# Kernel optimization log

Measured on AMD Instinct MI355X. Metric: run time of the kernel, lower is better.

## Reference

```python
import jax, jax.numpy as jnp
import numpy as np

B, D, H, W = 1, 16, 16, 16
C, NH = 528, 8
HD = C // NH      # 66
K = 32            # retrieved memories per token


def setup_inputs() -> dict:
    key = jax.random.key(0)
    ks = jax.random.split(key, 4)
    x = jax.random.normal(ks[0], (B, D, H, W, C), jnp.float32)
    # simulated knn_memory.search output: (B, heads, N, K, 2[k/v], head_dim)
    knn_kv = jax.random.normal(ks[1], (B, NH, D * H * W, K, 2, HD), jnp.float32)
    w_qkv = jax.random.normal(ks[2], (3 * C, C), jnp.float32) * 0.02
    b_qkv = jnp.zeros((3 * C,), jnp.float32)
    w_proj = jax.random.normal(ks[3], (C, C), jnp.float32) * 0.02
    b_proj = jnp.zeros((C,), jnp.float32)
    return {"x": x, "knn_kv": knn_kv, "w_qkv": w_qkv, "b_qkv": b_qkv,
            "w_proj": w_proj, "b_proj": b_proj, "num_heads": NH}


def _l2norm(t):
    # F.normalize(t, dim=-1): t / max(||t||_2, eps)
    n = jnp.linalg.norm(t, axis=-1, keepdims=True)
    return t / jnp.maximum(n, 1e-12)


def _forward(x, knn_kv, w_qkv, b_qkv, w_proj, b_proj, num_heads):
    Bb, Dd, Hh, Ww, Cc = x.shape
    N = Dd * Hh * Ww
    hd = Cc // num_heads
    scaling = hd ** -0.5
    qkv = x.reshape(Bb * N, Cc) @ w_qkv.T + b_qkv
    qkv = qkv.reshape(Bb, N, 3, num_heads, hd).transpose(2, 0, 3, 1, 4)  # (3,B,h,N,hd)
    q, k, v = qkv[0], qkv[1], qkv[2]
    q = _l2norm(q)
    k = _l2norm(k)
    knn_k = knn_kv[..., 0, :]   # (B,h,N,K,hd)
    knn_v = knn_kv[..., 1, :]
    k_comb = jnp.concatenate([knn_k, k[..., None, :]], axis=-2)  # (B,h,N,K+1,hd)
    v_comb = jnp.concatenate([knn_v, v[..., None, :]], axis=-2)
    attn = jnp.einsum('bhnd,bhnkd->bhnk', q, k_comb) * scaling
    attn = jax.nn.softmax(attn, axis=-1)  # stable softmax
    out = jnp.einsum('bhnk,bhnkd->bhnd', attn, v_comb)  # (B,h,N,hd)
    out = out.transpose(0, 2, 1, 3).reshape(Bb * N, num_heads * hd)
    out = out @ w_proj.T + b_proj
    return out.reshape(Bb, Dd, Hh, Ww, Cc)


def reference(x, knn_kv, w_qkv, b_qkv, w_proj, b_proj, num_heads):
    return _forward(x, knn_kv, w_qkv, b_qkv, w_proj, b_proj, num_heads)
```

## Files before the change

### kernel.cpp

```cpp
#include <hip/hip_runtime.h>
#include <hip/hip_bf16.h>
#include <math.h>

#define N_POS 4096
#define C_DIM 528
#define NHEAD 8
#define HDIM  66
#define KNN   32
#define CQKV  1584
#define KP    544
#define NP1   1664
#define NP2   640

typedef __attribute__((ext_vector_type(8))) short short8;
typedef __attribute__((ext_vector_type(4))) float f32x4;
typedef __hip_bfloat16 bf16;

__global__ __launch_bounds__(256) void convpad3_kernel(
    const float* __restrict__ x, const float* __restrict__ wq,
    const float* __restrict__ wp,
    bf16* __restrict__ xb, bf16* __restrict__ wqb, bf16* __restrict__ wpb)
{
    int b = blockIdx.x;
    const float* src; bf16* dst; int Nr;
    if (b < N_POS)            { src = x;  dst = xb;  Nr = N_POS; }
    else if (b < N_POS + NP1) { b -= N_POS; src = wq; dst = wqb; Nr = CQKV; }
    else                      { b -= N_POS + NP1; src = wp; dst = wpb; Nr = C_DIM; }
    for (int c = threadIdx.x; c < KP; c += 256) {
        float v = (b < Nr && c < C_DIM) ? src[(size_t)b * C_DIM + c] : 0.0f;
        dst[(size_t)b * KP + c] = __float2bfloat16(v);
    }
}

__global__ __launch_bounds__(256) void gemm_mfma_kernel(
    const bf16* __restrict__ A, const bf16* __restrict__ B,
    const float* __restrict__ bias, float* __restrict__ C,
    int Nreal, int ldc)
{
    __shared__ short8 As[512];
    __shared__ short8 Bs[512];

    const int tid  = threadIdx.x;
    const int lane = tid & 63;
    const int wid  = tid >> 6;
    const int bm = blockIdx.y * 128;
    const int bn = blockIdx.x * 128;

    const int r0 = tid >> 2;
    const int c0 = tid & 3;
    const bf16* Ag = A + (size_t)(bm + r0) * KP + c0 * 8;
    const bf16* Bg = B + (size_t)(bn + r0) * KP + c0 * 8;
    const size_t roff = (size_t)64 * KP;

    short8 a0 = *(const short8*)(Ag);
    short8 a1 = *(const short8*)(Ag + roff);
    short8 b0 = *(const short8*)(Bg);
    short8 b1 = *(const short8*)(Bg + roff);

    const int w0 = r0 * 4 + (c0 ^ (r0 & 3));
    const int w1 = w0 + 256;

    const int wm = (wid >> 1) * 64;
    const int wn = (wid & 1) * 64;
    const int arow = wm + (lane & 15);
    const int brow = wn + (lane & 15);
    const int apc  = lane >> 4;
    const int aslot = arow * 4 + (apc ^ (arow & 3));
    const int bslot = brow * 4 + (apc ^ (brow & 3));

    f32x4 acc[4][4];
    #pragma unroll
    for (int i = 0; i < 4; ++i)
        #pragma unroll
        for (int j = 0; j < 4; ++j)
            acc[i][j] = (f32x4){0.f, 0.f, 0.f, 0.f};

    for (int k0 = 0;; k0 += 32) {
        As[w0] = a0; As[w1] = a1;
        Bs[w0] = b0; Bs[w1] = b1;
        __syncthreads();
        if (k0 + 32 < KP) {
            const bf16* An = Ag + (k0 + 32);
            const bf16* Bn = Bg + (k0 + 32);
            a0 = *(const short8*)(An);
            a1 = *(const short8*)(An + roff);
            b0 = *(const short8*)(Bn);
            b1 = *(const short8*)(Bn + roff);
        }
        short8 af[4], bfr[4];
        #pragma unroll
        for (int f = 0; f < 4; ++f) af[f]  = As[aslot + f * 64];
        #pragma unroll
        for (int f = 0; f < 4; ++f) bfr[f] = Bs[bslot + f * 64];
        #pragma unroll
        for (int i = 0; i < 4; ++i)
            #pragma unroll
            for (int j = 0; j < 4; ++j)
                acc[i][j] = __builtin_amdgcn_mfma_f32_16x16x32_bf16(
                    af[i], bfr[j], acc[i][j], 0, 0, 0);
        if (k0 + 32 >= KP) break;
        __syncthreads();
    }

    #pragma unroll
    for (int i = 0; i < 4; ++i) {
        const int row = bm + wm + i * 16 + (lane >> 4) * 4;
        #pragma unroll
        for (int j = 0; j < 4; ++j) {
            const int col = bn + wn + j * 16 + (lane & 15);
            if (col < Nreal) {
                const float bv = bias[col];
                #pragma unroll
                for (int r = 0; r < 4; ++r)
                    C[(size_t)(row + r) * ldc + col] = acc[i][j][r] + bv;
            }
        }
    }
}

__global__ __launch_bounds__(256) void attn_kernel(
    const float* __restrict__ qkv, const float* __restrict__ knn,
    bf16* __restrict__ out)
{
    const float scaling = 0.12309149097933272f;

    const int bid = blockIdx.x;
    const int tid = threadIdx.x;
    const int g0  = bid << 1;
    const int h   = g0 >> 12;
    const int n0  = g0 & 4095;
    const int n1  = n0 + 1;

    __shared__ float s_knn[2][KNN * 132];
    __shared__ float s_qkv[2][3 * HDIM];
    __shared__ float s_dot[2][KNN + 1];
    __shared__ float s_sc[2][2];

    const float4* kb0 = (const float4*)(knn + (size_t)g0 * (KNN * 132));
    const float4* kb1 = kb0 + KNN * 33;
    float4 r0[4], r1[4];
    float4 e0 = {0.f, 0.f, 0.f, 0.f}, e1 = {0.f, 0.f, 0.f, 0.f};
    #pragma unroll
    for (int i = 0; i < 4; ++i) r0[i] = kb0[tid + 256 * i];
    if (tid < 32) e0 = kb0[1024 + tid];
    #pragma unroll
    for (int i = 0; i < 4; ++i) r1[i] = kb1[tid + 256 * i];
    if (tid < 32) e1 = kb1[1024 + tid];

    const float* qp0 = qkv + (size_t)n0 * CQKV + h * HDIM;
    const float* qp1 = qp0 + CQKV;
    float qv0 = 0.f, qv1 = 0.f;
    int part = tid / HDIM, d66 = tid - part * HDIM;
    if (tid < 3 * HDIM) {
        qv0 = qp0[part * C_DIM + d66];
        qv1 = qp1[part * C_DIM + d66];
    }

    float4* s40 = (float4*)s_knn[0];
    float4* s41 = (float4*)s_knn[1];
    #pragma unroll
    for (int i = 0; i < 4; ++i) s40[tid + 256 * i] = r0[i];
    if (tid < 32) s40[1024 + tid] = e0;
    #pragma unroll
    for (int i = 0; i < 4; ++i) s41[tid + 256 * i] = r1[i];
    if (tid < 32) s41[1024 + tid] = e1;
    if (tid < 3 * HDIM) {
        s_qkv[0][tid] = qv0;
        s_qkv[1][tid] = qv1;
    }
    __syncthreads();

    const int team  = tid >> 7;
    const int ttid  = tid & 127;
    const int twave = ttid >> 6;
    const int lane  = tid & 63;
    const float* kK = s_knn[team];
    const float* Q  = &s_qkv[team][0];
    const float* KS = &s_qkv[team][HDIM];

    if (twave == 0) {
        const int j = lane >> 1, l2 = lane & 1;
        const float* kr = kK + j * 132;
        float p = 0.f;
        #pragma unroll
        for (int d = 0; d < HDIM / 2; ++d) p += Q[2 * d + l2] * kr[2 * d + l2];
        p += __shfl_xor(p, 1);
        if (l2 == 0) s_dot[team][j] = p;
    } else {
        float aq, ak, qk;
        {
            float qd = Q[lane], kd = KS[lane];
            aq = qd * qd; ak = kd * kd; qk = qd * kd;
            if (lane < 2) {
                float q2 = Q[64 + lane], k2 = KS[64 + lane];
                aq += q2 * q2; ak += k2 * k2; qk += q2 * k2;
            }
        }
        #pragma unroll
        for (int off = 32; off; off >>= 1) {
            aq += __shfl_xor(aq, off);
            ak += __shfl_xor(ak, off);
            qk += __shfl_xor(qk, off);
        }
        if (lane == 0) {
            const float iq = 1.0f / fmaxf(sqrtf(aq), 1e-12f);
            const float ik = 1.0f / fmaxf(sqrtf(ak), 1e-12f);
            s_sc[team][0] = iq * scaling;
            s_sc[team][1] = qk * iq * ik * scaling;
        }
    }
    __syncthreads();

    if (twave == 0) {
        float x = -3.4e38f;
        if (lane < 32)       x = s_dot[team][lane] * s_sc[team][0];
        else if (lane == 32) x = s_sc[team][1];
        float m = x;
        #pragma unroll
        for (int off = 32; off; off >>= 1) m = fmaxf(m, __shfl_xor(m, off));
        float e = (lane < 33) ? expf(x - m) : 0.f;
        float s = e;
        #pragma unroll
        for (int off = 32; off; off >>= 1) s += __shfl_xor(s, off);
        if (lane < 33) s_dot[team][lane] = e / s;
    }
    __syncthreads();

    if (ttid < HDIM) {
        const int d = ttid;
        float acc = s_dot[team][KNN] * s_qkv[team][2 * HDIM + d];
        #pragma unroll 8
        for (int j = 0; j < KNN; ++j)
            acc += s_dot[team][j] * kK[j * 132 + HDIM + d];
        const int n = team ? n1 : n0;
        out[(size_t)n * KP + h * HDIM + d] = __float2bfloat16(acc);
    }
    if (h == 0) {
        if (tid < 16)
            out[(size_t)n0 * KP + C_DIM + tid] = __float2bfloat16(0.f);
        else if (tid < 32)
            out[(size_t)n1 * KP + C_DIM + (tid - 16)] = __float2bfloat16(0.f);
    }
}

extern "C" void kernel_launch(void* const* d_in, const int* in_sizes, int n_in,
                              void* d_out, int out_size, void* d_ws, size_t ws_size,
                              hipStream_t stream)
{
    const float* x      = (const float*)d_in[0];
    const float* knn_kv = (const float*)d_in[1];
    const float* w_qkv  = (const float*)d_in[2];
    const float* b_qkv  = (const float*)d_in[3];
    const float* w_proj = (const float*)d_in[4];
    const float* b_proj = (const float*)d_in[5];
    float* out = (float*)d_out;

    char* ws = (char*)d_ws;
    float* qkv = (float*)ws;
    bf16*  xb  = (bf16*)(ws + 25952256);
    bf16*  wqb = (bf16*)(ws + 25952256 + 4456448);
    bf16*  wpb = (bf16*)(ws + 25952256 + 4456448 + 1810432);
    bf16*  ab  = (bf16*)(ws + 25952256 + 4456448 + 1810432 + 696320);

    convpad3_kernel<<<N_POS + NP1 + NP2, 256, 0, stream>>>(x, w_qkv, w_proj, xb, wqb, wpb);

    gemm_mfma_kernel<<<dim3(NP1 / 128, N_POS / 128), 256, 0, stream>>>(
        xb, wqb, b_qkv, qkv, CQKV, CQKV);

    attn_kernel<<<dim3(NHEAD * N_POS / 2), 256, 0, stream>>>(qkv, knn_kv, ab);

    gemm_mfma_kernel<<<dim3(NP2 / 128, N_POS / 128), 256, 0, stream>>>(
        ab, wpb, b_proj, out, C_DIM, C_DIM);
}
```

Baseline: 171.0 us.

## Store QKV in bf16 and swizzle GEMM workgroup mapping across XCDs

The QKV GEMM now writes bf16 instead of fp32, halving the intermediate written by the GEMM and read by the attention kernel. Both GEMMs switch to a 1D grid with an XCD-aware swizzle so that consecutive tiles land on the same chiplet, aiming for better L2 reuse. Rounding q/k/v to bf16 adds precision error before normalization and softmax. The swizzle assumes the grid size is divisible by 8.

```diff
diff --git a/kernel.cpp b/kernel.cpp
--- a/kernel.cpp
+++ b/kernel.cpp
@@ -32,10 +32,11 @@
     }
 }
 
+template <bool BF16OUT>
 __global__ __launch_bounds__(256) void gemm_mfma_kernel(
     const bf16* __restrict__ A, const bf16* __restrict__ B,
-    const float* __restrict__ bias, float* __restrict__ C,
-    int Nreal, int ldc)
+    const float* __restrict__ bias, void* __restrict__ Cv,
+    int Nreal, int ldc, int nbx)
 {
     __shared__ short8 As[512];
     __shared__ short8 Bs[512];
@@ -43,8 +44,12 @@
     const int tid  = threadIdx.x;
     const int lane = tid & 63;
     const int wid  = tid >> 6;
-    const int bm = blockIdx.y * 128;
-    const int bn = blockIdx.x * 128;
+
+    const int nwg   = gridDim.x;
+    const int chunk = nwg >> 3;
+    const int swz   = (blockIdx.x & 7) * chunk + (blockIdx.x >> 3);
+    const int bm = (swz / nbx) * 128;
+    const int bn = (swz % nbx) * 128;
 
     const int r0 = tid >> 2;
     const int c0 = tid & 3;
@@ -111,15 +116,20 @@
             if (col < Nreal) {
                 const float bv = bias[col];
                 #pragma unroll
-                for (int r = 0; r < 4; ++r)
-                    C[(size_t)(row + r) * ldc + col] = acc[i][j][r] + bv;
+                for (int r = 0; r < 4; ++r) {
+                    const float o = acc[i][j][r] + bv;
+                    if (BF16OUT)
+                        ((bf16*)Cv)[(size_t)(row + r) * ldc + col] = __float2bfloat16(o);
+                    else
+                        ((float*)Cv)[(size_t)(row + r) * ldc + col] = o;
+                }
             }
         }
     }
 }
 
 __global__ __launch_bounds__(256) void attn_kernel(
-    const float* __restrict__ qkv, const float* __restrict__ knn,
+    const bf16* __restrict__ qkv, const float* __restrict__ knn,
     bf16* __restrict__ out)
 {
     const float scaling = 0.12309149097933272f;
@@ -147,13 +157,13 @@
     for (int i = 0; i < 4; ++i) r1[i] = kb1[tid + 256 * i];
     if (tid < 32) e1 = kb1[1024 + tid];
 
-    const float* qp0 = qkv + (size_t)n0 * CQKV + h * HDIM;
-    const float* qp1 = qp0 + CQKV;
+    const bf16* qp0 = qkv + (size_t)n0 * CQKV + h * HDIM;
+    const bf16* qp1 = qp0 + CQKV;
     float qv0 = 0.f, qv1 = 0.f;
     int part = tid / HDIM, d66 = tid - part * HDIM;
     if (tid < 3 * HDIM) {
-        qv0 = qp0[part * C_DIM + d66];
-        qv1 = qp1[part * C_DIM + d66];
+        qv0 = __bfloat162float(qp0[part * C_DIM + d66]);
+        qv1 = __bfloat162float(qp1[part * C_DIM + d66]);
     }
 
     float4* s40 = (float4*)s_knn[0];
@@ -256,19 +266,19 @@
     float* out = (float*)d_out;
 
     char* ws = (char*)d_ws;
-    float* qkv = (float*)ws;
-    bf16*  xb  = (bf16*)(ws + 25952256);
-    bf16*  wqb = (bf16*)(ws + 25952256 + 4456448);
-    bf16*  wpb = (bf16*)(ws + 25952256 + 4456448 + 1810432);
-    bf16*  ab  = (bf16*)(ws + 25952256 + 4456448 + 1810432 + 696320);
+    bf16* qkvb = (bf16*)ws;
+    bf16* xb   = (bf16*)(ws + 12976128);
+    bf16* wqb  = (bf16*)(ws + 12976128 + 4456448);
+    bf16* wpb  = (bf16*)(ws + 12976128 + 4456448 + 1810432);
+    bf16* ab   = (bf16*)(ws + 12976128 + 4456448 + 1810432 + 696320);
 
     convpad3_kernel<<<N_POS + NP1 + NP2, 256, 0, stream>>>(x, w_qkv, w_proj, xb, wqb, wpb);
 
-    gemm_mfma_kernel<<<dim3(NP1 / 128, N_POS / 128), 256, 0, stream>>>(
-        xb, wqb, b_qkv, qkv, CQKV, CQKV);
-
-    attn_kernel<<<dim3(NHEAD * N_POS / 2), 256, 0, stream>>>(qkv, knn_kv, ab);
-
-    gemm_mfma_kernel<<<dim3(NP2 / 128, N_POS / 128), 256, 0, stream>>>(
-        ab, wpb, b_proj, out, C_DIM, C_DIM);
-}
+    gemm_mfma_kernel<true><<<dim3((NP1 / 128) * (N_POS / 128)), 256, 0, stream>>>(
+        xb, wqb, b_qkv, qkvb, CQKV, CQKV, NP1 / 128);
+
+    attn_kernel<<<dim3(NHEAD * N_POS / 2), 256, 0, stream>>>(qkvb, knn_kv, ab);
+
+    gemm_mfma_kernel<false><<<dim3((NP2 / 128) * (N_POS / 128)), 256, 0, stream>>>(
+        ab, wpb, b_proj, out, C_DIM, C_DIM, NP2 / 128);
+}
```

Result: no change. 171.8 us (+0.5%).
